# Kernel optimization log

Measured on AMD Instinct MI355X. Metric: run time of the kernel, lower is better.

The kernel has to match this reference:

```python
import jax, jax.numpy as jnp
from jax import lax
import numpy as np

ALPHA = 100.0  # NetVLAD beta

def _avg_pool2(x):
    # AvgPool2d(2, stride=2) on NCHW
    s = lax.reduce_window(x, 0.0, lax.add, (1, 1, 2, 2), (1, 1, 2, 2), 'VALID')
    return s * 0.25

def _conv3x3(x, w, b):
    y = lax.conv_general_dilated(x, w, (1, 1), 'SAME',
                                 dimension_numbers=('NCHW', 'OIHW', 'NCHW'))
    return y + b[None, :, None, None]

def _l2norm(v, axis):
    return v / jnp.maximum(jnp.linalg.norm(v, axis=axis, keepdims=True), 1e-12)


def setup_inputs() -> dict:
    key = jax.random.key(0)
    ks = jax.random.split(key, 10)
    N, H, W = 16, 512, 512
    K, D = 64, 16          # clusters, NetVLAD feature dim (conv2 out channels)
    T, E, Hd = 64, 300, 512  # caption len, emb dim (rnn_inp=rnn_out), rnn_hid
    img = jax.random.normal(ks[0], (N, 3, H, W), jnp.float32)
    cap = jax.random.normal(ks[1], (N, T, E), jnp.float32)
    conv1_w = jax.random.normal(ks[2], (4, 3, 3, 3), jnp.float32) * 0.1
    conv1_b = jnp.zeros((4,), jnp.float32)
    conv2_w = jax.random.normal(ks[3], (16, 4, 3, 3), jnp.float32) * 0.1
    conv2_b = jnp.zeros((16,), jnp.float32)
    centroids = jax.random.uniform(ks[4], (K, D), jnp.float32)  # torch.rand init
    nv_w = 2.0 * ALPHA * centroids                     # 1x1 conv weight, squeezed [K,D]
    nv_b = -ALPHA * jnp.linalg.norm(centroids, axis=1)  # [K]
    fc_w = jax.random.normal(ks[5], (Hd, K * D), jnp.float32) * 0.02
    fc_b = jnp.zeros((Hd,), jnp.float32)
    hid_w = jax.random.normal(ks[6], (Hd, E + Hd), jnp.float32) * 0.02
    hid_b = jnp.zeros((Hd,), jnp.float32)
    out_w = jax.random.normal(ks[7], (E, Hd), jnp.float32) * 0.02
    out_b = jnp.zeros((E,), jnp.float32)
    return dict(img=img, cap=cap, conv1_w=conv1_w, conv1_b=conv1_b,
                conv2_w=conv2_w, conv2_b=conv2_b, centroids=centroids,
                nv_w=nv_w, nv_b=nv_b, fc_w=fc_w, fc_b=fc_b,
                hid_w=hid_w, hid_b=hid_b, out_w=out_w, out_b=out_b)


def reference(img, cap, conv1_w, conv1_b, conv2_w, conv2_b, centroids,
              nv_w, nv_b, fc_w, fc_b, hid_w, hid_b, out_w, out_b):
    # CNN encoder
    x = jax.nn.relu(_conv3x3(img, conv1_w, conv1_b))
    x = _avg_pool2(x)
    x = jax.nn.relu(_conv3x3(x, conv2_w, conv2_b))
    x = _avg_pool2(x)                      # [N, 16, 128, 128]
    N, C = x.shape[0], x.shape[1]
    xf = x.reshape(N, C, -1)               # [N, C, HW]
    # NetVLAD: 1x1 conv -> softmax over clusters
    soft_assign = jnp.einsum('kc,nch->nkh', nv_w, xf) + nv_b[None, :, None]
    soft_assign = jax.nn.softmax(soft_assign, axis=1)  # [N, K, HW]
    # algebraic two-matmul form of sum_hw a[n,k,hw]*(x[n,c,hw]-centroids[k,c])
    a_sum = soft_assign.sum(axis=-1)                      # [N, K]
    vlad = jnp.einsum('nkh,nch->nkc', soft_assign, xf)    # [N, K, C]
    vlad = vlad - a_sum[:, :, None] * centroids[None]     # [N, K, C]
    vlad = _l2norm(vlad, axis=2)
    vlad = vlad.reshape(N, -1)
    vlad = _l2norm(vlad, axis=1)
    features = vlad @ fc_w.T + fc_b                        # [N, rnn_hid]
    # RNN decoder on sample 0
    feat0 = features[0]
    cap0 = cap[0]                                          # [T, E]

    def step(carry, x_t):
        h, x_in = carry
        comb = jnp.concatenate([x_in, h])
        h_new = jax.nn.sigmoid(hid_w @ comb + hid_b)
        y = jax.nn.sigmoid(out_w @ h_new + out_b)
        return (h_new, x_t), y

    (_, ys) = lax.scan(step, (feat0, cap0[0]), cap0[1:])
    output = jnp.concatenate([cap0[:1], ys], axis=0)       # [T, E]
    loss = jnp.mean((output - cap0) ** 2)
    return loss
```

## Files before the change

### kernel.cpp

```cpp
#include <hip/hip_runtime.h>
#include <math.h>


#define HPOISON 0xAAAAAAAAu

__device__ __forceinline__ float sigmoidf_(float x) {
  return 1.0f / (1.0f + __expf(-x));
}

__global__ __launch_bounds__(256) void k_conv1(const float* __restrict__ img,
                                               const float* __restrict__ w,
                                               const float* __restrict__ b,
                                               float* __restrict__ p1) {
  int idx = blockIdx.x * 256 + threadIdx.x;
  int ox = idx & 255;
  int oy = (idx >> 8) & 255;
  int c  = idx >> 16;
  __shared__ float wsh[27];
  __shared__ float bsh;
  if (threadIdx.x < 27) wsh[threadIdx.x] = w[c * 27 + threadIdx.x];
  if (threadIdx.x == 0) bsh = b[c];
  __syncthreads();
  int y0 = oy * 2 - 1, x0 = ox * 2 - 1;
  float a00, a01, a10, a11;
  a00 = a01 = a10 = a11 = bsh;
  #pragma unroll
  for (int ci = 0; ci < 3; ++ci) {
    float P[4][4];
    #pragma unroll
    for (int j = 0; j < 4; ++j) {
      int y = y0 + j;
      #pragma unroll
      for (int i = 0; i < 4; ++i) {
        int x = x0 + i;
        bool ok = ((unsigned)y < 512u) && ((unsigned)x < 512u);
        P[j][i] = ok ? img[ci * 262144 + y * 512 + x] : 0.0f;
      }
    }
    #pragma unroll
    for (int ky = 0; ky < 3; ++ky) {
      #pragma unroll
      for (int kx = 0; kx < 3; ++kx) {
        float wv = wsh[ci * 9 + ky * 3 + kx];
        a00 = fmaf(wv, P[ky][kx],         a00);
        a01 = fmaf(wv, P[ky][kx + 1],     a01);
        a10 = fmaf(wv, P[ky + 1][kx],     a10);
        a11 = fmaf(wv, P[ky + 1][kx + 1], a11);
      }
    }
  }
  p1[idx] = 0.25f * (fmaxf(a00, 0.f) + fmaxf(a01, 0.f) +
                     fmaxf(a10, 0.f) + fmaxf(a11, 0.f));
}

#define PS_STRIDE 65
#define XS_STRIDE 20
__global__ __launch_bounds__(256, 1) void k_conv2vlad(const float* __restrict__ p1,
                                                      const float* __restrict__ w2,
                                                      const float* __restrict__ b2,
                                                      const float* __restrict__ nvw,
                                                      const float* __restrict__ nvb,
                                                      float* __restrict__ vacc,
                                                      float* __restrict__ asum) {
  __shared__ __align__(16) float ps[128 * PS_STRIDE];
  __shared__ __align__(16) float xs[128 * XS_STRIDE];
  __shared__ float wsh[1024];
  __shared__ float bsh[64];
  __shared__ float aS[256];
  __shared__ float cw[576];
  __shared__ float cb[16];
  int tid = threadIdx.x;
  for (int i = tid; i < 1024; i += 256) wsh[i] = nvw[i];
  if (tid < 64) bsh[tid] = nvb[tid];
  for (int i = tid; i < 576; i += 256) cw[i] = w2[i];
  if (tid < 16) cb[tid] = b2[tid];
  __syncthreads();

  int ox = tid & 127;
  int oyl = tid >> 7;
  int oy = blockIdx.x * 2 + oyl;
  int y0 = oy * 2 - 1, x0 = ox * 2 - 1;
  float a[16][4];
  #pragma unroll
  for (int oc = 0; oc < 16; ++oc) {
    float bb = cb[oc];
    a[oc][0] = bb; a[oc][1] = bb; a[oc][2] = bb; a[oc][3] = bb;
  }
  #pragma unroll
  for (int ci = 0; ci < 4; ++ci) {
    float P[4][4];
    #pragma unroll
    for (int j = 0; j < 4; ++j) {
      int y = y0 + j;
      #pragma unroll
      for (int i = 0; i < 4; ++i) {
        int x = x0 + i;
        bool ok = ((unsigned)y < 256u) && ((unsigned)x < 256u);
        P[j][i] = ok ? p1[ci * 65536 + y * 256 + x] : 0.0f;
      }
    }
    #pragma unroll
    for (int oc = 0; oc < 16; ++oc) {
      #pragma unroll
      for (int ky = 0; ky < 3; ++ky) {
        #pragma unroll
        for (int kx = 0; kx < 3; ++kx) {
          float wv = cw[oc * 36 + ci * 9 + ky * 3 + kx];
          a[oc][0] = fmaf(wv, P[ky][kx],         a[oc][0]);
          a[oc][1] = fmaf(wv, P[ky][kx + 1],     a[oc][1]);
          a[oc][2] = fmaf(wv, P[ky + 1][kx],     a[oc][2]);
          a[oc][3] = fmaf(wv, P[ky + 1][kx + 1], a[oc][3]);
        }
      }
    }
  }
  float x[16];
  #pragma unroll
  for (int oc = 0; oc < 16; ++oc)
    x[oc] = 0.25f * (fmaxf(a[oc][0], 0.f) + fmaxf(a[oc][1], 0.f) +
                     fmaxf(a[oc][2], 0.f) + fmaxf(a[oc][3], 0.f));

  float p[64];
  float m = -1e30f;
  #pragma unroll
  for (int k = 0; k < 64; ++k) {
    float acc = bsh[k];
    #pragma unroll
    for (int c = 0; c < 16; ++c) acc = fmaf(wsh[k * 16 + c], x[c], acc);
    p[k] = acc;
    m = fmaxf(m, acc);
  }
  float s = 0.f;
  #pragma unroll
  for (int k = 0; k < 64; ++k) { p[k] = __expf(p[k] - m); s += p[k]; }
  float inv = 1.0f / s;
  #pragma unroll
  for (int k = 0; k < 64; ++k) p[k] *= inv;

  int q = tid >> 6, k = tid & 63;
  float acc[16];
  #pragma unroll
  for (int c = 0; c < 16; ++c) acc[c] = 0.f;
  float accA = 0.f;

  for (int pass = 0; pass < 2; ++pass) {
    __syncthreads();
    if ((tid >> 7) == pass) {
      int tt = tid & 127;
      #pragma unroll
      for (int kk = 0; kk < 64; ++kk) ps[tt * PS_STRIDE + kk] = p[kk];
      #pragma unroll
      for (int c = 0; c < 16; ++c) xs[tt * XS_STRIDE + c] = x[c];
    }
    __syncthreads();
    #pragma unroll
    for (int j = 0; j < 32; ++j) {
      int tt = q * 32 + j;
      float pv = ps[tt * PS_STRIDE + k];
      accA += pv;
      const float4* xv = (const float4*)(xs + tt * XS_STRIDE);
      #pragma unroll
      for (int c4 = 0; c4 < 4; ++c4) {
        float4 xx = xv[c4];
        acc[c4 * 4 + 0] = fmaf(pv, xx.x, acc[c4 * 4 + 0]);
        acc[c4 * 4 + 1] = fmaf(pv, xx.y, acc[c4 * 4 + 1]);
        acc[c4 * 4 + 2] = fmaf(pv, xx.z, acc[c4 * 4 + 2]);
        acc[c4 * 4 + 3] = fmaf(pv, xx.w, acc[c4 * 4 + 3]);
      }
    }
  }
  __syncthreads();
  float* red = ps;
  #pragma unroll
  for (int c = 0; c < 16; ++c) red[tid * 16 + c] = acc[c];
  aS[tid] = accA;
  __syncthreads();
  if (q == 0) {
    float aa = aS[k] + aS[64 + k] + aS[128 + k] + aS[192 + k];
    atomicAdd(&asum[k], aa);
  }
  int k2 = tid >> 2;
  int cg = (tid & 3) * 4;
  #pragma unroll
  for (int cc = 0; cc < 4; ++cc) {
    int c = cg + cc;
    float v = red[(0 * 64 + k2) * 16 + c] + red[(1 * 64 + k2) * 16 + c] +
              red[(2 * 64 + k2) * 16 + c] + red[(3 * 64 + k2) * 16 + c];
    atomicAdd(&vacc[k2 * 16 + c], v);
  }
}

__global__ __launch_bounds__(512) void k_featU(const float* __restrict__ hid_w,
                                               const float* __restrict__ hid_b,
                                               const float* __restrict__ cap,
                                               const float* __restrict__ vacc,
                                               const float* __restrict__ asum,
                                               const float* __restrict__ cent,
                                               const float* __restrict__ fcw,
                                               const float* __restrict__ fcb,
                                               float* __restrict__ U,
                                               float* __restrict__ feat) {
  int tid = threadIdx.x;
  if (blockIdx.x < 63) {
    int t = blockIdx.x;
    __shared__ __align__(16) float csh[300];
    if (tid < 300) csh[tid] = cap[t * 300 + tid];
    __syncthreads();
    float acc = hid_b[tid];
    const float4* w4 = (const float4*)(hid_w + tid * 812);
    const float4* c4 = (const float4*)csh;
    #pragma unroll 5
    for (int i = 0; i < 75; ++i) {
      float4 aa = w4[i]; float4 xx = c4[i];
      acc = fmaf(aa.x, xx.x, acc); acc = fmaf(aa.y, xx.y, acc);
      acc = fmaf(aa.z, xx.z, acc); acc = fmaf(aa.w, xx.w, acc);
    }
    U[t * 512 + tid] = acc;
    return;
  }
  int q = blockIdx.x - 63;
  __shared__ __align__(16) float v[1024];
  __shared__ float rn[64];
  __shared__ float red[9];
  for (int i = tid; i < 1024; i += 512)
    v[i] = vacc[i] - asum[i >> 4] * cent[i];
  __syncthreads();
  if (tid < 64) {
    float ss = 0.f;
    #pragma unroll
    for (int c = 0; c < 16; ++c) { float xx = v[tid * 16 + c]; ss = fmaf(xx, xx, ss); }
    rn[tid] = fmaxf(sqrtf(ss), 1e-12f);
  }
  __syncthreads();
  float gs = 0.f;
  for (int i = tid; i < 1024; i += 512) {
    float nv = v[i] / rn[i >> 4];
    v[i] = nv;
    gs = fmaf(nv, nv, gs);
  }
  #pragma unroll
  for (int o = 32; o > 0; o >>= 1) gs += __shfl_down(gs, o);
  int wv = tid >> 6, lane = tid & 63;
  if (lane == 0) red[wv] = gs;
  __syncthreads();
  if (tid == 0) {
    float tot = 0.f;
    #pragma unroll
    for (int qq = 0; qq < 8; ++qq) tot += red[qq];
    red[8] = 1.0f / fmaxf(sqrtf(tot), 1e-12f);
  }
  __syncthreads();
  float invg = red[8];
  int r = q * 64 + (tid >> 3);
  int cch = tid & 7;
  float acc = 0.f;
  const float4* fw4 = (const float4*)(fcw + r * 1024 + cch * 128);
  const float4* v4  = (const float4*)(v + cch * 128);
  #pragma unroll 4
  for (int i = 0; i < 32; ++i) {
    float4 aa = fw4[i]; float4 xx = v4[i];
    acc = fmaf(aa.x, xx.x, acc); acc = fmaf(aa.y, xx.y, acc);
    acc = fmaf(aa.z, xx.z, acc); acc = fmaf(aa.w, xx.w, acc);
  }
  acc += __shfl_down(acc, 4, 8);
  acc += __shfl_down(acc, 2, 8);
  acc += __shfl_down(acc, 1, 8);
  if (cch == 0) feat[r] = fmaf(invg, acc, fcb[r]);
}

__global__ __launch_bounds__(256, 1) void k_rnn(const float* __restrict__ hid_w,
                                                const float* __restrict__ U,
                                                const float* __restrict__ feat,
                                                float* __restrict__ H) {
  const int b = blockIdx.x;
  const int tid = threadIdx.x;
  const int wv = tid >> 6;
  const int lane = tid & 63;
  const int row = b * 64 + lane;
  const int colbase = wv * 128;
  float4 wr[32];
  const float4* wp = (const float4*)(hid_w + row * 812 + 300 + colbase);
  #pragma unroll
  for (int i = 0; i < 32; ++i) wr[i] = wp[i];
  __shared__ __align__(16) float hsh[512];
  __shared__ float part[4][64];
  unsigned int* Hu = (unsigned int*)H;
  for (int t = 0; t < 63; ++t) {
    float uval = (wv == 0) ? U[t * 512 + row] : 0.f;
    if (t == 0) {
      hsh[tid] = feat[tid];
      hsh[tid + 256] = feat[tid + 256];
    } else {
      const unsigned int* src = Hu + (t - 1) * 512;
      unsigned int a0, a1;
      do {
        a0 = __hip_atomic_load(src + tid, __ATOMIC_RELAXED,
                               __HIP_MEMORY_SCOPE_AGENT);
      } while (a0 == HPOISON);
      do {
        a1 = __hip_atomic_load(src + tid + 256, __ATOMIC_RELAXED,
                               __HIP_MEMORY_SCOPE_AGENT);
      } while (a1 == HPOISON);
      hsh[tid] = __uint_as_float(a0);
      hsh[tid + 256] = __uint_as_float(a1);
    }
    __syncthreads();
    float acc = 0.0f;
    #pragma unroll
    for (int i = 0; i < 32; ++i) {
      float4 hv = *(const float4*)(hsh + colbase + i * 4);
      acc = fmaf(wr[i].x, hv.x, acc);
      acc = fmaf(wr[i].y, hv.y, acc);
      acc = fmaf(wr[i].z, hv.z, acc);
      acc = fmaf(wr[i].w, hv.w, acc);
    }
    part[wv][lane] = acc;
    __syncthreads();
    if (wv == 0) {
      float pre = part[0][lane] + part[1][lane] + part[2][lane] +
                  part[3][lane] + uval;
      float hn = sigmoidf_(pre);
      __hip_atomic_store(Hu + t * 512 + row, __float_as_uint(hn),
                         __ATOMIC_RELAXED, __HIP_MEMORY_SCOPE_AGENT);
    }
  }
}

__global__ __launch_bounds__(512) void k_loss(const float* __restrict__ outw,
                                              const float* __restrict__ outb,
                                              const float* __restrict__ H,
                                              const float* __restrict__ cap,
                                              float* __restrict__ loss) {
  int t = blockIdx.x;
  int tid = threadIdx.x;
  __shared__ __align__(16) float hsh[512];
  __shared__ float red[8];
  hsh[tid] = H[t * 512 + tid];
  __syncthreads();
  float se = 0.f;
  if (tid < 300) {
    float acc = outb[tid];
    const float4* w4 = (const float4*)(outw + tid * 512);
    const float4* h4 = (const float4*)hsh;
    #pragma unroll 4
    for (int i = 0; i < 128; ++i) {
      float4 aa = w4[i]; float4 xx = h4[i];
      acc = fmaf(aa.x, xx.x, acc); acc = fmaf(aa.y, xx.y, acc);
      acc = fmaf(aa.z, xx.z, acc); acc = fmaf(aa.w, xx.w, acc);
    }
    float y = sigmoidf_(acc);
    float d = y - cap[(t + 1) * 300 + tid];
    se = d * d;
  }
  #pragma unroll
  for (int o = 32; o > 0; o >>= 1) se += __shfl_down(se, o);
  if ((tid & 63) == 0) red[tid >> 6] = se;
  __syncthreads();
  if (tid == 0) {
    float tot = 0.f;
    #pragma unroll
    for (int qq = 0; qq < 8; ++qq) tot += red[qq];
    atomicAdd(loss, tot * (1.0f / 19200.0f));
  }
}

extern "C" void kernel_launch(void* const* d_in, const int* in_sizes, int n_in,
                              void* d_out, int out_size, void* d_ws, size_t ws_size,
                              hipStream_t stream) {
  (void)in_sizes; (void)n_in; (void)out_size; (void)ws_size;
  const float* img  = (const float*)d_in[0];
  const float* cap  = (const float*)d_in[1];
  const float* c1w  = (const float*)d_in[2];
  const float* c1b  = (const float*)d_in[3];
  const float* c2w  = (const float*)d_in[4];
  const float* c2b  = (const float*)d_in[5];
  const float* cent = (const float*)d_in[6];
  const float* nvw  = (const float*)d_in[7];
  const float* nvb  = (const float*)d_in[8];
  const float* fcw  = (const float*)d_in[9];
  const float* fcb  = (const float*)d_in[10];
  const float* hidw = (const float*)d_in[11];
  const float* hidb = (const float*)d_in[12];
  const float* outw = (const float*)d_in[13];
  const float* outb = (const float*)d_in[14];

  float* ws   = (float*)d_ws;
  float* p1   = ws;
  float* vacc = ws + 262144;
  float* asum = ws + 263168;
  float* feat = ws + 263232;
  float* U    = ws + 263744;
  float* H    = ws + 296000;

  hipMemsetAsync(vacc, 0, (1024 + 64) * sizeof(float), stream);
  hipMemsetAsync(H, 0xAA, 63 * 512 * sizeof(float), stream);
  hipMemsetAsync(d_out, 0, sizeof(float), stream);

  k_conv1<<<1024, 256, 0, stream>>>(img, c1w, c1b, p1);
  k_conv2vlad<<<64, 256, 0, stream>>>(p1, c2w, c2b, nvw, nvb, vacc, asum);
  k_featU<<<71, 512, 0, stream>>>(hidw, hidb, cap, vacc, asum, cent,
                                  fcw, fcb, U, feat);
  k_rnn<<<8, 256, 0, stream>>>(hidw, U, feat, H);
  k_loss<<<63, 512, 0, stream>>>(outw, outb, H, cap, (float*)d_out);
}
```

Before: 296.2 us.

## Fold memsets and U precompute into conv1 launch; make RNN step wave-local

The three memset calls and the caption-side U projection move into extra blocks of the conv1 kernel, which removes separate launches and overlaps the U work with the convolution. The old featU kernel shrinks to just the FC part. The RNN kernel now has each wave own 16 rows, with 4 lanes per row splitting the columns. Each wave keeps its own copy of h and reduces with shuffles, so the block-level __syncthreads and the shared partial-sum exchange are replaced by wave barriers. The cost is redundant polling of H by every wave and wider per-lane atomic loads.

```diff
diff --git a/kernel.cpp b/kernel.cpp
--- a/kernel.cpp
+++ b/kernel.cpp
@@ -8,49 +8,90 @@
   return 1.0f / (1.0f + __expf(-x));
 }
 
-__global__ __launch_bounds__(256) void k_conv1(const float* __restrict__ img,
+__global__ __launch_bounds__(256) void k_front(const float* __restrict__ img,
                                                const float* __restrict__ w,
                                                const float* __restrict__ b,
-                                               float* __restrict__ p1) {
-  int idx = blockIdx.x * 256 + threadIdx.x;
-  int ox = idx & 255;
-  int oy = (idx >> 8) & 255;
-  int c  = idx >> 16;
-  __shared__ float wsh[27];
-  __shared__ float bsh;
-  if (threadIdx.x < 27) wsh[threadIdx.x] = w[c * 27 + threadIdx.x];
-  if (threadIdx.x == 0) bsh = b[c];
-  __syncthreads();
-  int y0 = oy * 2 - 1, x0 = ox * 2 - 1;
-  float a00, a01, a10, a11;
-  a00 = a01 = a10 = a11 = bsh;
-  #pragma unroll
-  for (int ci = 0; ci < 3; ++ci) {
-    float P[4][4];
-    #pragma unroll
-    for (int j = 0; j < 4; ++j) {
-      int y = y0 + j;
-      #pragma unroll
-      for (int i = 0; i < 4; ++i) {
-        int x = x0 + i;
-        bool ok = ((unsigned)y < 512u) && ((unsigned)x < 512u);
-        P[j][i] = ok ? img[ci * 262144 + y * 512 + x] : 0.0f;
-      }
-    }
-    #pragma unroll
-    for (int ky = 0; ky < 3; ++ky) {
-      #pragma unroll
-      for (int kx = 0; kx < 3; ++kx) {
-        float wv = wsh[ci * 9 + ky * 3 + kx];
-        a00 = fmaf(wv, P[ky][kx],         a00);
-        a01 = fmaf(wv, P[ky][kx + 1],     a01);
-        a10 = fmaf(wv, P[ky + 1][kx],     a10);
-        a11 = fmaf(wv, P[ky + 1][kx + 1], a11);
-      }
-    }
-  }
-  p1[idx] = 0.25f * (fmaxf(a00, 0.f) + fmaxf(a01, 0.f) +
-                     fmaxf(a10, 0.f) + fmaxf(a11, 0.f));
+                                               const float* __restrict__ hid_w,
+                                               const float* __restrict__ hid_b,
+                                               const float* __restrict__ cap,
+                                               float* __restrict__ p1,
+                                               float* __restrict__ U,
+                                               float* __restrict__ vacc,
+                                               float* __restrict__ asum,
+                                               float* __restrict__ H,
+                                               float* __restrict__ out) {
+  int bx = blockIdx.x;
+  int tid = threadIdx.x;
+  if (bx < 1024) {
+    int idx = bx * 256 + tid;
+    int ox = idx & 255;
+    int oy = (idx >> 8) & 255;
+    int c  = idx >> 16;
+    __shared__ float wsh[27];
+    __shared__ float bsh;
+    if (tid < 27) wsh[tid] = w[c * 27 + tid];
+    if (tid == 0) bsh = b[c];
+    __syncthreads();
+    int y0 = oy * 2 - 1, x0 = ox * 2 - 1;
+    float a00, a01, a10, a11;
+    a00 = a01 = a10 = a11 = bsh;
+    #pragma unroll
+    for (int ci = 0; ci < 3; ++ci) {
+      float P[4][4];
+      #pragma unroll
+      for (int j = 0; j < 4; ++j) {
+        int y = y0 + j;
+        #pragma unroll
+        for (int i = 0; i < 4; ++i) {
+          int x = x0 + i;
+          bool ok = ((unsigned)y < 512u) && ((unsigned)x < 512u);
+          P[j][i] = ok ? img[ci * 262144 + y * 512 + x] : 0.0f;
+        }
+      }
+      #pragma unroll
+      for (int ky = 0; ky < 3; ++ky) {
+        #pragma unroll
+        for (int kx = 0; kx < 3; ++kx) {
+          float wv = wsh[ci * 9 + ky * 3 + kx];
+          a00 = fmaf(wv, P[ky][kx],         a00);
+          a01 = fmaf(wv, P[ky][kx + 1],     a01);
+          a10 = fmaf(wv, P[ky + 1][kx],     a10);
+          a11 = fmaf(wv, P[ky + 1][kx + 1], a11);
+        }
+      }
+    }
+    p1[idx] = 0.25f * (fmaxf(a00, 0.f) + fmaxf(a01, 0.f) +
+                       fmaxf(a10, 0.f) + fmaxf(a11, 0.f));
+    return;
+  }
+  if (bx < 1087) {
+    int t = bx - 1024;
+    __shared__ __align__(16) float csh[300];
+    if (tid < 256) csh[tid] = cap[t * 300 + tid];
+    if (tid < 44) csh[256 + tid] = cap[t * 300 + 256 + tid];
+    __syncthreads();
+    #pragma unroll
+    for (int rr = 0; rr < 2; ++rr) {
+      int r = tid + rr * 256;
+      float acc = hid_b[r];
+      const float4* w4 = (const float4*)(hid_w + r * 812);
+      const float4* c4 = (const float4*)csh;
+      #pragma unroll 5
+      for (int i = 0; i < 75; ++i) {
+        float4 aa = w4[i]; float4 xx = c4[i];
+        acc = fmaf(aa.x, xx.x, acc); acc = fmaf(aa.y, xx.y, acc);
+        acc = fmaf(aa.z, xx.z, acc); acc = fmaf(aa.w, xx.w, acc);
+      }
+      U[t * 512 + r] = acc;
+    }
+    return;
+  }
+  for (int i = tid; i < 1024; i += 256) vacc[i] = 0.f;
+  if (tid < 64) asum[tid] = 0.f;
+  if (tid == 0) out[0] = 0.f;
+  uint4* Hu4 = (uint4*)H;
+  uint4 pz = make_uint4(HPOISON, HPOISON, HPOISON, HPOISON);
+  for (int i = tid; i < (63 * 512) / 4; i += 256) Hu4[i] = pz;
 }
 
 #define PS_STRIDE 65
@@ -190,35 +231,14 @@
   }
 }
 
-__global__ __launch_bounds__(512) void k_featU(const float* __restrict__ hid_w,
-                                               const float* __restrict__ hid_b,
-                                               const float* __restrict__ cap,
-                                               const float* __restrict__ vacc,
-                                               const float* __restrict__ asum,
-                                               const float* __restrict__ cent,
-                                               const float* __restrict__ fcw,
-                                               const float* __restrict__ fcb,
-                                               float* __restrict__ U,
-                                               float* __restrict__ feat) {
+__global__ __launch_bounds__(512) void k_fc(const float* __restrict__ vacc,
+                                            const float* __restrict__ asum,
+                                            const float* __restrict__ cent,
+                                            const float* __restrict__ fcw,
+                                            const float* __restrict__ fcb,
+                                            float* __restrict__ feat) {
   int tid = threadIdx.x;
-  if (blockIdx.x < 63) {
-    int t = blockIdx.x;
-    __shared__ __align__(16) float csh[300];
-    if (tid < 300) csh[tid] = cap[t * 300 + tid];
-    __syncthreads();
-    float acc = hid_b[tid];
-    const float4* w4 = (const float4*)(hid_w + tid * 812);
-    const float4* c4 = (const float4*)csh;
-    #pragma unroll 5
-    for (int i = 0; i < 75; ++i) {
-      float4 aa = w4[i]; float4 xx = c4[i];
-      acc = fmaf(aa.x, xx.x, acc); acc = fmaf(aa.y, xx.y, acc);
-      acc = fmaf(aa.z, xx.z, acc); acc = fmaf(aa.w, xx.w, acc);
-    }
-    U[t * 512 + tid] = acc;
-    return;
-  }
-  int q = blockIdx.x - 63;
+  int q = blockIdx.x;
   __shared__ __align__(16) float v[1024];
   __shared__ float rn[64];
   __shared__ float red[9];
@@ -272,57 +292,61 @@
                                                 const float* __restrict__ U,
                                                 const float* __restrict__ feat,
                                                 float* __restrict__ H) {
-  const int b = blockIdx.x;
   const int tid = threadIdx.x;
   const int wv = tid >> 6;
   const int lane = tid & 63;
-  const int row = b * 64 + lane;
-  const int colbase = wv * 128;
+  const int r = lane >> 2;
+  const int cg = lane & 3;
+  const int row = blockIdx.x * 64 + wv * 16 + r;
+  const int colbase = cg * 128;
   float4 wr[32];
   const float4* wp = (const float4*)(hid_w + row * 812 + 300 + colbase);
   #pragma unroll
   for (int i = 0; i < 32; ++i) wr[i] = wp[i];
-  __shared__ __align__(16) float hsh[512];
-  __shared__ float part[4][64];
+  __shared__ __align__(16) float hsh[4][512];
+  float* hw = hsh[wv];
   unsigned int* Hu = (unsigned int*)H;
+  const int pbase = lane * 8;
   for (int t = 0; t < 63; ++t) {
-    float uval = (wv == 0) ? U[t * 512 + row] : 0.f;
+    float uval = U[t * 512 + row];
     if (t == 0) {
-      hsh[tid] = feat[tid];
-      hsh[tid + 256] = feat[tid + 256];
+      float4 f0 = *(const float4*)(feat + pbase);
+      float4 f1 = *(const float4*)(feat + pbase + 4);
+      *(float4*)(hw + pbase) = f0;
+      *(float4*)(hw + pbase + 4) = f1;
     } else {
-      const unsigned int* src = Hu + (t - 1) * 512;
-      unsigned int a0, a1;
+      const unsigned int* src = Hu + (t - 1) * 512 + pbase;
+      unsigned int a[8];
+      bool again;
       do {
-        a0 = __hip_atomic_load(src + tid, __ATOMIC_RELAXED,
-                               __HIP_MEMORY_SCOPE_AGENT);
-      } while (a0 == HPOISON);
-      do {
-        a1 = __hip_atomic_load(src + tid + 256, __ATOMIC_RELAXED,
-                               __HIP_MEMORY_SCOPE_AGENT);
-      } while (a1 == HPOISON);
-      hsh[tid] = __uint_as_float(a0);
-      hsh[tid + 256] = __uint_as_float(a1);
-    }
-    __syncthreads();
+        #pragma unroll
+        for (int j = 0; j < 8; ++j)
+          a[j] = __hip_atomic_load(src + j, __ATOMIC_RELAXED,
+                                   __HIP_MEMORY_SCOPE_AGENT);
+        again = false;
+        #pragma unroll
+        for (int j = 0; j < 8; ++j) again = again || (a[j] == HPOISON);
+      } while (again);
+      #pragma unroll
+      for (int j = 0; j < 8; ++j) hw[pbase + j] = __uint_as_float(a[j]);
+    }
+    __builtin_amdgcn_wave_barrier();
     float acc = 0.0f;
     #pragma unroll
     for (int i = 0; i < 32; ++i) {
-      float4 hv = *(const float4*)(hsh + colbase + i * 4);
+      float4 hv = *(const float4*)(hw + colbase + i * 4);
       acc = fmaf(wr[i].x, hv.x, acc);
       acc = fmaf(wr[i].y, hv.y, acc);
       acc = fmaf(wr[i].z, hv.z, acc);
       acc = fmaf(wr[i].w, hv.w, acc);
     }
-    part[wv][lane] = acc;
-    __syncthreads();
-    if (wv == 0) {
-      float pre = part[0][lane] + part[1][lane] + part[2][lane] +
-                  part[3][lane] + uval;
-      float hn = sigmoidf_(pre);
+    acc += __shfl_xor(acc, 1);
+    acc += __shfl_xor(acc, 2);
+    float hn = sigmoidf_(acc + uval);
+    if (cg == 0)
       __hip_atomic_store(Hu + t * 512 + row, __float_as_uint(hn),
                          __ATOMIC_RELAXED, __HIP_MEMORY_SCOPE_AGENT);
-    }
+    __builtin_amdgcn_wave_barrier();
   }
 }
 
@@ -392,14 +416,10 @@
   float* U    = ws + 263744;
   float* H    = ws + 296000;
 
-  hipMemsetAsync(vacc, 0, (1024 + 64) * sizeof(float), stream);
-  hipMemsetAsync(H, 0xAA, 63 * 512 * sizeof(float), stream);
-  hipMemsetAsync(d_out, 0, sizeof(float), stream);
-
-  k_conv1<<<1024, 256, 0, stream>>>(img, c1w, c1b, p1);
+  k_front<<<1088, 256, 0, stream>>>(img, c1w, c1b, hidw, hidb, cap,
+                                    p1, U, vacc, asum, H, (float*)d_out);
   k_conv2vlad<<<64, 256, 0, stream>>>(p1, c2w, c2b, nvw, nvb, vacc, asum);
-  k_featU<<<71, 512, 0, stream>>>(hidw, hidb, cap, vacc, asum, cent,
-                                  fcw, fcb, U, feat);
+  k_fc<<<8, 512, 0, stream>>>(vacc, asum, cent, fcw, fcb, feat);
   k_rnn<<<8, 256, 0, stream>>>(hidw, U, feat, H);
   k_loss<<<63, 512, 0, stream>>>(outw, outb, H, cap, (float*)d_out);
 }
```

New measurement: 391.2 us. 32.1% more time.

## Fuse whole pipeline into one persistent kernel with flag-based inter-block sync

Applied to the files above, without the earlier changes.

Replaces the three memsets and five kernel launches with a single 256-block persistent kernel whose blocks take different roles: conv1 workers, conv2+VLAD workers, feature projection, input projection, RNN recurrence and loss. Ordering between roles uses a magic ready flag, completion counters, and poison-value polling on global buffers in place of kernel boundaries. This removes launch and memset overhead and lets the U-projection and loss work overlap the serial RNN. In exchange it depends on every block being co-resident, since spinning blocks would otherwise deadlock, and the flag protocol is fragile because the magic flag is never reset between calls.

```diff
diff --git a/kernel.cpp b/kernel.cpp
--- a/kernel.cpp
+++ b/kernel.cpp
@@ -2,365 +2,446 @@
 #include <math.h>
 
 
-#define HPOISON 0xAAAAAAAAu
+#define POISON 0xAAAAAAAAu
+#define MAGIC  0x13579BDFu
 
 __device__ __forceinline__ float sigmoidf_(float x) {
   return 1.0f / (1.0f + __expf(-x));
 }
-
-__global__ __launch_bounds__(256) void k_conv1(const float* __restrict__ img,
-                                               const float* __restrict__ w,
-                                               const float* __restrict__ b,
-                                               float* __restrict__ p1) {
-  int idx = blockIdx.x * 256 + threadIdx.x;
-  int ox = idx & 255;
-  int oy = (idx >> 8) & 255;
-  int c  = idx >> 16;
-  __shared__ float wsh[27];
-  __shared__ float bsh;
-  if (threadIdx.x < 27) wsh[threadIdx.x] = w[c * 27 + threadIdx.x];
-  if (threadIdx.x == 0) bsh = b[c];
-  __syncthreads();
-  int y0 = oy * 2 - 1, x0 = ox * 2 - 1;
-  float a00, a01, a10, a11;
-  a00 = a01 = a10 = a11 = bsh;
-  #pragma unroll
-  for (int ci = 0; ci < 3; ++ci) {
-    float P[4][4];
-    #pragma unroll
-    for (int j = 0; j < 4; ++j) {
-      int y = y0 + j;
-      #pragma unroll
-      for (int i = 0; i < 4; ++i) {
-        int x = x0 + i;
-        bool ok = ((unsigned)y < 512u) && ((unsigned)x < 512u);
-        P[j][i] = ok ? img[ci * 262144 + y * 512 + x] : 0.0f;
-      }
-    }
-    #pragma unroll
-    for (int ky = 0; ky < 3; ++ky) {
-      #pragma unroll
-      for (int kx = 0; kx < 3; ++kx) {
-        float wv = wsh[ci * 9 + ky * 3 + kx];
-        a00 = fmaf(wv, P[ky][kx],         a00);
-        a01 = fmaf(wv, P[ky][kx + 1],     a01);
-        a10 = fmaf(wv, P[ky + 1][kx],     a10);
-        a11 = fmaf(wv, P[ky + 1][kx + 1], a11);
-      }
-    }
+__device__ __forceinline__ unsigned uld(const unsigned* p) {
+  return __hip_atomic_load(p, __ATOMIC_RELAXED, __HIP_MEMORY_SCOPE_AGENT);
+}
+__device__ __forceinline__ float fld(const float* p) {
+  return __hip_atomic_load(p, __ATOMIC_RELAXED, __HIP_MEMORY_SCOPE_AGENT);
+}
+__device__ __forceinline__ void fst(float* p, float v) {
+  __hip_atomic_store(p, v, __ATOMIC_RELAXED, __HIP_MEMORY_SCOPE_AGENT);
+}
+__device__ __forceinline__ void ust(unsigned* p, unsigned v) {
+  __hip_atomic_store(p, v, __ATOMIC_RELAXED, __HIP_MEMORY_SCOPE_AGENT);
+}
+
+__global__ __launch_bounds__(256, 1)
+void k_fused(const float* __restrict__ img,  const float* __restrict__ cap,
+             const float* __restrict__ c1w,  const float* __restrict__ c1b,
+             const float* __restrict__ c2w,  const float* __restrict__ c2b,
+             const float* __restrict__ cent, const float* __restrict__ nvw,
+             const float* __restrict__ nvb,  const float* __restrict__ fcw,
+             const float* __restrict__ fcb,  const float* __restrict__ hidw,
+             const float* __restrict__ hidb, const float* __restrict__ outw,
+             const float* __restrict__ outb,
+             float* __restrict__ p1,   float* __restrict__ vacc,
+             float* __restrict__ asum, float* __restrict__ feat,
+             float* __restrict__ U,    float* __restrict__ H,
+             unsigned* __restrict__ flags, float* __restrict__ loss) {
+  __shared__ __align__(16) float smem[12832];
+  const int bx  = blockIdx.x;
+  const int tid = threadIdx.x;
+  unsigned* flag_ready = flags + 0;
+  unsigned* conv_done  = flags + 1;
+  unsigned* vlad_done  = flags + 2;
+
+  if (bx < 8) {
+    if (bx == 0) {
+      for (int i = tid; i < 1024; i += 256) fst(vacc + i, 0.f);
+      if (tid < 64) fst(asum + tid, 0.f);
+      if (tid == 0) { fst(loss, 0.f); ust(conv_done, 0u); ust(vlad_done, 0u); }
+      unsigned* Uu = (unsigned*)U;
+      unsigned* Hu = (unsigned*)H;
+      unsigned* Fu = (unsigned*)feat;
+      for (int i = tid; i < 63 * 512; i += 256) ust(Uu + i, POISON);
+      for (int i = tid; i < 63 * 512; i += 256) ust(Hu + i, POISON);
+      if (tid < 256) { ust(Fu + tid, POISON); ust(Fu + tid + 256, POISON); }
+      __syncthreads();
+      if (tid == 0)
+        __hip_atomic_store(flag_ready, MAGIC, __ATOMIC_RELEASE,
+                           __HIP_MEMORY_SCOPE_AGENT);
+    }
+    const int r   = tid >> 2;
+    const int cg  = tid & 3;
+    const int row = bx * 64 + r;
+    float4 wr[32];
+    const float4* wp = (const float4*)(hidw + row * 812 + 300 + cg * 128);
+    #pragma unroll
+    for (int i = 0; i < 32; ++i) wr[i] = wp[i];
+    if (bx != 0) {
+      if (tid == 0) {
+        while (__hip_atomic_load(flag_ready, __ATOMIC_ACQUIRE,
+                                 __HIP_MEMORY_SCOPE_AGENT) != MAGIC)
+          __builtin_amdgcn_s_sleep(2);
+      }
+      __syncthreads();
+    }
+    float* buf0 = smem;
+    float* buf1 = smem + 544;
+    const int w0 = (tid >> 7) * 136 + (tid & 127);
+    const int w1 = ((tid + 256) >> 7) * 136 + ((tid + 256) & 127);
+    const int wown = (row >> 7) * 136 + (row & 127);
+    const bool own0 = ((tid >> 6) == bx);
+    const bool own1 = (((tid + 256) >> 6) == bx);
+    {
+      const unsigned* fu = (const unsigned*)feat;
+      unsigned f0, f1;
+      do {
+        f0 = uld(fu + tid);
+        f1 = uld(fu + tid + 256);
+      } while (f0 == POISON || f1 == POISON);
+      buf0[w0] = __uint_as_float(f0);
+      buf0[w1] = __uint_as_float(f1);
+    }
+    unsigned upat = 0;
+    if (cg == 0) upat = uld((const unsigned*)(U + row));
+    __syncthreads();
+    unsigned* Hu = (unsigned*)H;
+    for (int t = 0; t < 63; ++t) {
+      const float* bufc = (t & 1) ? buf1 : buf0;
+      const float* rb = bufc + cg * 136;
+      float acc = 0.f;
+      #pragma unroll
+      for (int i = 0; i < 32; ++i) {
+        float4 h4 = *(const float4*)(rb + i * 4);
+        acc = fmaf(wr[i].x, h4.x, acc);
+        acc = fmaf(wr[i].y, h4.y, acc);
+        acc = fmaf(wr[i].z, h4.z, acc);
+        acc = fmaf(wr[i].w, h4.w, acc);
+      }
+      acc += __shfl_xor(acc, 1);
+      acc += __shfl_xor(acc, 2);
+      float hn = 0.f;
+      if (cg == 0) {
+        while (upat == POISON) upat = uld((const unsigned*)(U + t * 512 + row));
+        hn = sigmoidf_(acc + __uint_as_float(upat));
+        fst(H + t * 512 + row, hn);
+      }
+      if (t < 62) {
+        float* bufn = (t & 1) ? buf0 : buf1;
+        if (cg == 0) {
+          bufn[wown] = hn;
+          upat = uld((const unsigned*)(U + (t + 1) * 512 + row));
+        }
+        const unsigned* src = Hu + t * 512;
+        unsigned a0 = 0, a1 = 0;
+        do {
+          if (!own0) a0 = uld(src + tid);
+          if (!own1) a1 = uld(src + tid + 256);
+        } while ((!own0 && a0 == POISON) || (!own1 && a1 == POISON));
+        if (!own0) bufn[w0] = __uint_as_float(a0);
+        if (!own1) bufn[w1] = __uint_as_float(a1);
+        __syncthreads();
+      }
+    }
+    return;
   }
-  p1[idx] = 0.25f * (fmaxf(a00, 0.f) + fmaxf(a01, 0.f) +
-                     fmaxf(a10, 0.f) + fmaxf(a11, 0.f));
-}
-
-#define PS_STRIDE 65
-#define XS_STRIDE 20
-__global__ __launch_bounds__(256, 1) void k_conv2vlad(const float* __restrict__ p1,
-                                                      const float* __restrict__ w2,
-                                                      const float* __restrict__ b2,
-                                                      const float* __restrict__ nvw,
-                                                      const float* __restrict__ nvb,
-                                                      float* __restrict__ vacc,
-                                                      float* __restrict__ asum) {
-  __shared__ __align__(16) float ps[128 * PS_STRIDE];
-  __shared__ __align__(16) float xs[128 * XS_STRIDE];
-  __shared__ float wsh[1024];
-  __shared__ float bsh[64];
-  __shared__ float aS[256];
-  __shared__ float cw[576];
-  __shared__ float cb[16];
-  int tid = threadIdx.x;
-  for (int i = tid; i < 1024; i += 256) wsh[i] = nvw[i];
-  if (tid < 64) bsh[tid] = nvb[tid];
-  for (int i = tid; i < 576; i += 256) cw[i] = w2[i];
-  if (tid < 16) cb[tid] = b2[tid];
-  __syncthreads();
-
-  int ox = tid & 127;
-  int oyl = tid >> 7;
-  int oy = blockIdx.x * 2 + oyl;
-  int y0 = oy * 2 - 1, x0 = ox * 2 - 1;
-  float a[16][4];
-  #pragma unroll
-  for (int oc = 0; oc < 16; ++oc) {
-    float bb = cb[oc];
-    a[oc][0] = bb; a[oc][1] = bb; a[oc][2] = bb; a[oc][3] = bb;
+
+  if (bx < 71) {
+    const int t = bx - 8;
+    if (tid == 0) {
+      while (__hip_atomic_load(flag_ready, __ATOMIC_ACQUIRE,
+                               __HIP_MEMORY_SCOPE_AGENT) != MAGIC)
+        __builtin_amdgcn_s_sleep(8);
+    }
+    __syncthreads();
+    float* csh = smem;
+    if (tid < 256) csh[tid] = cap[t * 300 + tid];
+    if (tid < 44) csh[256 + tid] = cap[t * 300 + 256 + tid];
+    __syncthreads();
+    #pragma unroll
+    for (int rr = 0; rr < 2; ++rr) {
+      int rrow = tid + rr * 256;
+      float acc = hidb[rrow];
+      const float4* w4 = (const float4*)(hidw + rrow * 812);
+      const float4* c4 = (const float4*)csh;
+      #pragma unroll 5
+      for (int i = 0; i < 75; ++i) {
+        float4 aa = w4[i]; float4 xx = c4[i];
+        acc = fmaf(aa.x, xx.x, acc); acc = fmaf(aa.y, xx.y, acc);
+        acc = fmaf(aa.z, xx.z, acc); acc = fmaf(aa.w, xx.w, acc);
+      }
+      fst(U + t * 512 + rrow, acc);
+    }
+    __syncthreads();
+    const unsigned* Hu = (const unsigned*)H;
+    if (tid == 0) {
+      while (uld(Hu + (size_t)t * 512) == POISON) __builtin_amdgcn_s_sleep(64);
+    }
+    __syncthreads();
+    float* hsh = smem;
+    {
+      const unsigned* src = Hu + (size_t)t * 512;
+      unsigned a0, a1;
+      do {
+        a0 = uld(src + tid);
+        a1 = uld(src + tid + 256);
+      } while (a0 == POISON || a1 == POISON);
+      hsh[tid] = __uint_as_float(a0);
+      hsh[tid + 256] = __uint_as_float(a1);
+    }
+    __syncthreads();
+    float se = 0.f;
+    #pragma unroll
+    for (int rr = 0; rr < 2; ++rr) {
+      int orow = tid + rr * 256;
+      if (orow < 300) {
+        float acc = outb[orow];
+        const float4* w4 = (const float4*)(outw + orow * 512);
+        const float4* h4 = (const float4*)hsh;
+        #pragma unroll 4
+        for (int i = 0; i < 128; ++i) {
+          float4 aa = w4[i]; float4 xx = h4[i];
+          acc = fmaf(aa.x, xx.x, acc); acc = fmaf(aa.y, xx.y, acc);
+          acc = fmaf(aa.z, xx.z, acc); acc = fmaf(aa.w, xx.w, acc);
+        }
+        float y = sigmoidf_(acc);
+        float d = y - cap[(t + 1) * 300 + orow];
+        se = fmaf(d, d, se);
+      }
+    }
+    #pragma unroll
+    for (int o = 32; o > 0; o >>= 1) se += __shfl_down(se, o);
+    float* red = smem + 512;
+    if ((tid & 63) == 0) red[tid >> 6] = se;
+    __syncthreads();
+    if (tid == 0) {
+      float tot = red[0] + red[1] + red[2] + red[3];
+      atomicAdd(loss, tot * (1.0f / 19200.0f));
+    }
+    return;
   }
-  #pragma unroll
-  for (int ci = 0; ci < 4; ++ci) {
-    float P[4][4];
-    #pragma unroll
-    for (int j = 0; j < 4; ++j) {
-      int y = y0 + j;
-      #pragma unroll
-      for (int i = 0; i < 4; ++i) {
-        int x = x0 + i;
-        bool ok = ((unsigned)y < 256u) && ((unsigned)x < 256u);
-        P[j][i] = ok ? p1[ci * 65536 + y * 256 + x] : 0.0f;
-      }
-    }
-    #pragma unroll
-    for (int oc = 0; oc < 16; ++oc) {
-      #pragma unroll
-      for (int ky = 0; ky < 3; ++ky) {
-        #pragma unroll
-        for (int kx = 0; kx < 3; ++kx) {
-          float wv = cw[oc * 36 + ci * 9 + ky * 3 + kx];
-          a[oc][0] = fmaf(wv, P[ky][kx],         a[oc][0]);
-          a[oc][1] = fmaf(wv, P[ky][kx + 1],     a[oc][1]);
-          a[oc][2] = fmaf(wv, P[ky + 1][kx],     a[oc][2]);
-          a[oc][3] = fmaf(wv, P[ky + 1][kx + 1], a[oc][3]);
-        }
-      }
-    }
-  }
-  float x[16];
-  #pragma unroll
-  for (int oc = 0; oc < 16; ++oc)
-    x[oc] = 0.25f * (fmaxf(a[oc][0], 0.f) + fmaxf(a[oc][1], 0.f) +
-                     fmaxf(a[oc][2], 0.f) + fmaxf(a[oc][3], 0.f));
-
-  float p[64];
-  float m = -1e30f;
-  #pragma unroll
-  for (int k = 0; k < 64; ++k) {
-    float acc = bsh[k];
-    #pragma unroll
-    for (int c = 0; c < 16; ++c) acc = fmaf(wsh[k * 16 + c], x[c], acc);
-    p[k] = acc;
-    m = fmaxf(m, acc);
-  }
-  float s = 0.f;
-  #pragma unroll
-  for (int k = 0; k < 64; ++k) { p[k] = __expf(p[k] - m); s += p[k]; }
-  float inv = 1.0f / s;
-  #pragma unroll
-  for (int k = 0; k < 64; ++k) p[k] *= inv;
-
-  int q = tid >> 6, k = tid & 63;
-  float acc[16];
-  #pragma unroll
-  for (int c = 0; c < 16; ++c) acc[c] = 0.f;
-  float accA = 0.f;
-
-  for (int pass = 0; pass < 2; ++pass) {
-    __syncthreads();
-    if ((tid >> 7) == pass) {
-      int tt = tid & 127;
-      #pragma unroll
-      for (int kk = 0; kk < 64; ++kk) ps[tt * PS_STRIDE + kk] = p[kk];
-      #pragma unroll
-      for (int c = 0; c < 16; ++c) xs[tt * XS_STRIDE + c] = x[c];
-    }
-    __syncthreads();
-    #pragma unroll
-    for (int j = 0; j < 32; ++j) {
-      int tt = q * 32 + j;
-      float pv = ps[tt * PS_STRIDE + k];
-      accA += pv;
-      const float4* xv = (const float4*)(xs + tt * XS_STRIDE);
-      #pragma unroll
-      for (int c4 = 0; c4 < 4; ++c4) {
-        float4 xx = xv[c4];
-        acc[c4 * 4 + 0] = fmaf(pv, xx.x, acc[c4 * 4 + 0]);
-        acc[c4 * 4 + 1] = fmaf(pv, xx.y, acc[c4 * 4 + 1]);
-        acc[c4 * 4 + 2] = fmaf(pv, xx.z, acc[c4 * 4 + 2]);
-        acc[c4 * 4 + 3] = fmaf(pv, xx.w, acc[c4 * 4 + 3]);
-      }
-    }
-  }
-  __syncthreads();
-  float* red = ps;
-  #pragma unroll
-  for (int c = 0; c < 16; ++c) red[tid * 16 + c] = acc[c];
-  aS[tid] = accA;
-  __syncthreads();
-  if (q == 0) {
-    float aa = aS[k] + aS[64 + k] + aS[128 + k] + aS[192 + k];
-    atomicAdd(&asum[k], aa);
-  }
-  int k2 = tid >> 2;
-  int cg = (tid & 3) * 4;
-  #pragma unroll
-  for (int cc = 0; cc < 4; ++cc) {
-    int c = cg + cc;
-    float v = red[(0 * 64 + k2) * 16 + c] + red[(1 * 64 + k2) * 16 + c] +
-              red[(2 * 64 + k2) * 16 + c] + red[(3 * 64 + k2) * 16 + c];
-    atomicAdd(&vacc[k2 * 16 + c], v);
-  }
-}
-
-__global__ __launch_bounds__(512) void k_featU(const float* __restrict__ hid_w,
-                                               const float* __restrict__ hid_b,
-                                               const float* __restrict__ cap,
-                                               const float* __restrict__ vacc,
-                                               const float* __restrict__ asum,
-                                               const float* __restrict__ cent,
-                                               const float* __restrict__ fcw,
-                                               const float* __restrict__ fcb,
-                                               float* __restrict__ U,
-                                               float* __restrict__ feat) {
-  int tid = threadIdx.x;
-  if (blockIdx.x < 63) {
-    int t = blockIdx.x;
-    __shared__ __align__(16) float csh[300];
-    if (tid < 300) csh[tid] = cap[t * 300 + tid];
-    __syncthreads();
-    float acc = hid_b[tid];
-    const float4* w4 = (const float4*)(hid_w + tid * 812);
-    const float4* c4 = (const float4*)csh;
-    #pragma unroll 5
-    for (int i = 0; i < 75; ++i) {
-      float4 aa = w4[i]; float4 xx = c4[i];
+
+  if (bx < 79) {
+    const int q = bx - 71;
+    if (tid == 0) {
+      while (uld(vlad_done) != 64u) __builtin_amdgcn_s_sleep(8);
+    }
+    __syncthreads();
+    float* v  = smem;
+    float* rn = smem + 1024;
+    float* fr = smem + 1088;
+    for (int i = tid; i < 1024; i += 256)
+      v[i] = fld(vacc + i) - fld(asum + (i >> 4)) * cent[i];
+    __syncthreads();
+    if (tid < 64) {
+      float ss = 0.f;
+      #pragma unroll
+      for (int c = 0; c < 16; ++c) { float xx = v[tid * 16 + c]; ss = fmaf(xx, xx, ss); }
+      rn[tid] = fmaxf(sqrtf(ss), 1e-12f);
+    }
+    __syncthreads();
+    float gs = 0.f;
+    for (int i = tid; i < 1024; i += 256) {
+      float nv = v[i] / rn[i >> 4];
+      v[i] = nv;
+      gs = fmaf(nv, nv, gs);
+    }
+    #pragma unroll
+    for (int o = 32; o > 0; o >>= 1) gs += __shfl_down(gs, o);
+    if ((tid & 63) == 0) fr[tid >> 6] = gs;
+    __syncthreads();
+    if (tid == 0) {
+      float tot = fr[0] + fr[1] + fr[2] + fr[3];
+      fr[8] = 1.0f / fmaxf(sqrtf(tot), 1e-12f);
+    }
+    __syncthreads();
+    float invg = fr[8];
+    int row = q * 64 + (tid >> 2);
+    int cg = tid & 3;
+    float acc = 0.f;
+    const float4* fw4 = (const float4*)(fcw + row * 1024 + cg * 256);
+    const float4* v4  = (const float4*)(v + cg * 256);
+    #pragma unroll 4
+    for (int i = 0; i < 64; ++i) {
+      float4 aa = fw4[i]; float4 xx = v4[i];
       acc = fmaf(aa.x, xx.x, acc); acc = fmaf(aa.y, xx.y, acc);
       acc = fmaf(aa.z, xx.z, acc); acc = fmaf(aa.w, xx.w, acc);
     }
-    U[t * 512 + tid] = acc;
+    acc += __shfl_xor(acc, 1);
+    acc += __shfl_xor(acc, 2);
+    if (cg == 0) fst(feat + row, fmaf(invg, acc, fcb[row]));
     return;
   }
-  int q = blockIdx.x - 63;
-  __shared__ __align__(16) float v[1024];
-  __shared__ float rn[64];
-  __shared__ float red[9];
-  for (int i = tid; i < 1024; i += 512)
-    v[i] = vacc[i] - asum[i >> 4] * cent[i];
-  __syncthreads();
-  if (tid < 64) {
-    float ss = 0.f;
-    #pragma unroll
-    for (int c = 0; c < 16; ++c) { float xx = v[tid * 16 + c]; ss = fmaf(xx, xx, ss); }
-    rn[tid] = fmaxf(sqrtf(ss), 1e-12f);
+
+  if (bx < 143) {
+    const int vb = bx - 79;
+    float* ps  = smem;
+    float* xs  = smem + 8320;
+    float* wsh = smem + 10880;
+    float* bsh = smem + 11904;
+    float* aS  = smem + 11968;
+    float* cw  = smem + 12224;
+    float* cb  = smem + 12800;
+    for (int i = tid; i < 1024; i += 256) wsh[i] = nvw[i];
+    if (tid < 64) bsh[tid] = nvb[tid];
+    for (int i = tid; i < 576; i += 256) cw[i] = c2w[i];
+    if (tid < 16) cb[tid] = c2b[tid];
+    if (tid == 0) {
+      while (uld(conv_done) != 113u) __builtin_amdgcn_s_sleep(4);
+    }
+    __syncthreads();
+    int ox = tid & 127;
+    int oy = vb * 2 + (tid >> 7);
+    int y0 = oy * 2 - 1, x0 = ox * 2 - 1;
+    float a[16][4];
+    #pragma unroll
+    for (int oc = 0; oc < 16; ++oc) {
+      float bb = cb[oc];
+      a[oc][0] = bb; a[oc][1] = bb; a[oc][2] = bb; a[oc][3] = bb;
+    }
+    #pragma unroll
+    for (int ci = 0; ci < 4; ++ci) {
+      float P[4][4];
+      #pragma unroll
+      for (int j = 0; j < 4; ++j) {
+        int y = y0 + j;
+        #pragma unroll
+        for (int i = 0; i < 4; ++i) {
+          int x = x0 + i;
+          bool ok = ((unsigned)y < 256u) && ((unsigned)x < 256u);
+          P[j][i] = ok ? fld(p1 + ci * 65536 + y * 256 + x) : 0.0f;
+        }
+      }
+      #pragma unroll
+      for (int oc = 0; oc < 16; ++oc) {
+        #pragma unroll
+        for (int ky = 0; ky < 3; ++ky) {
+          #pragma unroll
+          for (int kx = 0; kx < 3; ++kx) {
+            float wv = cw[oc * 36 + ci * 9 + ky * 3 + kx];
+            a[oc][0] = fmaf(wv, P[ky][kx],         a[oc][0]);
+            a[oc][1] = fmaf(wv, P[ky][kx + 1],     a[oc][1]);
+            a[oc][2] = fmaf(wv, P[ky + 1][kx],     a[oc][2]);
+            a[oc][3] = fmaf(wv, P[ky + 1][kx + 1], a[oc][3]);
+          }
+        }
+      }
+    }
+    float x[16];
+    #pragma unroll
+    for (int oc = 0; oc < 16; ++oc)
+      x[oc] = 0.25f * (fmaxf(a[oc][0], 0.f) + fmaxf(a[oc][1], 0.f) +
+                       fmaxf(a[oc][2], 0.f) + fmaxf(a[oc][3], 0.f));
+    float p[64];
+    float m = -1e30f;
+    #pragma unroll
+    for (int k = 0; k < 64; ++k) {
+      float acc = bsh[k];
+      #pragma unroll
+      for (int c = 0; c < 16; ++c) acc = fmaf(wsh[k * 16 + c], x[c], acc);
+      p[k] = acc;
+      m = fmaxf(m, acc);
+    }
+    float s = 0.f;
+    #pragma unroll
+    for (int k = 0; k < 64; ++k) { p[k] = __expf(p[k] - m); s += p[k]; }
+    float inv = 1.0f / s;
+    #pragma unroll
+    for (int k = 0; k < 64; ++k) p[k] *= inv;
+
+    int q = tid >> 6, k = tid & 63;
+    float acc[16];
+    #pragma unroll
+    for (int c = 0; c < 16; ++c) acc[c] = 0.f;
+    float accA = 0.f;
+    for (int pass = 0; pass < 2; ++pass) {
+      __syncthreads();
+      if ((tid >> 7) == pass) {
+        int tt = tid & 127;
+        #pragma unroll
+        for (int kk = 0; kk < 64; ++kk) ps[tt * 65 + kk] = p[kk];
+        #pragma unroll
+        for (int c = 0; c < 16; ++c) xs[tt * 20 + c] = x[c];
+      }
+      __syncthreads();
+      #pragma unroll
+      for (int j = 0; j < 32; ++j) {
+        int tt = q * 32 + j;
+        float pv = ps[tt * 65 + k];
+        accA += pv;
+        const float4* xv = (const float4*)(xs + tt * 20);
+        #pragma unroll
+        for (int c4 = 0; c4 < 4; ++c4) {
+          float4 xx = xv[c4];
+          acc[c4 * 4 + 0] = fmaf(pv, xx.x, acc[c4 * 4 + 0]);
+          acc[c4 * 4 + 1] = fmaf(pv, xx.y, acc[c4 * 4 + 1]);
+          acc[c4 * 4 + 2] = fmaf(pv, xx.z, acc[c4 * 4 + 2]);
+          acc[c4 * 4 + 3] = fmaf(pv, xx.w, acc[c4 * 4 + 3]);
+        }
+      }
+    }
+    __syncthreads();
+    float* red = ps;
+    #pragma unroll
+    for (int c = 0; c < 16; ++c) red[tid * 16 + c] = acc[c];
+    aS[tid] = accA;
+    __syncthreads();
+    if (q == 0) {
+      float aa = aS[k] + aS[64 + k] + aS[128 + k] + aS[192 + k];
+      atomicAdd(&asum[k], aa);
+    }
+    int k2 = tid >> 2;
+    int cgc = (tid & 3) * 4;
+    #pragma unroll
+    for (int cc = 0; cc < 4; ++cc) {
+      int c = cgc + cc;
+      float vv = red[(0 * 64 + k2) * 16 + c] + red[(1 * 64 + k2) * 16 + c] +
+                 red[(2 * 64 + k2) * 16 + c] + red[(3 * 64 + k2) * 16 + c];
+      atomicAdd(&vacc[k2 * 16 + c], vv);
+    }
+    __syncthreads();
+    if (tid == 0)
+      __hip_atomic_fetch_add(vlad_done, 1u, __ATOMIC_RELAXED,
+                             __HIP_MEMORY_SCOPE_AGENT);
+    return;
   }
-  __syncthreads();
-  float gs = 0.f;
-  for (int i = tid; i < 1024; i += 512) {
-    float nv = v[i] / rn[i >> 4];
-    v[i] = nv;
-    gs = fmaf(nv, nv, gs);
-  }
-  #pragma unroll
-  for (int o = 32; o > 0; o >>= 1) gs += __shfl_down(gs, o);
-  int wv = tid >> 6, lane = tid & 63;
-  if (lane == 0) red[wv] = gs;
-  __syncthreads();
-  if (tid == 0) {
-    float tot = 0.f;
-    #pragma unroll
-    for (int qq = 0; qq < 8; ++qq) tot += red[qq];
-    red[8] = 1.0f / fmaxf(sqrtf(tot), 1e-12f);
-  }
-  __syncthreads();
-  float invg = red[8];
-  int r = q * 64 + (tid >> 3);
-  int cch = tid & 7;
-  float acc = 0.f;
-  const float4* fw4 = (const float4*)(fcw + r * 1024 + cch * 128);
-  const float4* v4  = (const float4*)(v + cch * 128);
-  #pragma unroll 4
-  for (int i = 0; i < 32; ++i) {
-    float4 aa = fw4[i]; float4 xx = v4[i];
-    acc = fmaf(aa.x, xx.x, acc); acc = fmaf(aa.y, xx.y, acc);
-    acc = fmaf(aa.z, xx.z, acc); acc = fmaf(aa.w, xx.w, acc);
-  }
-  acc += __shfl_down(acc, 4, 8);
-  acc += __shfl_down(acc, 2, 8);
-  acc += __shfl_down(acc, 1, 8);
-  if (cch == 0) feat[r] = fmaf(invg, acc, fcb[r]);
-}
-
-__global__ __launch_bounds__(256, 1) void k_rnn(const float* __restrict__ hid_w,
-                                                const float* __restrict__ U,
-                                                const float* __restrict__ feat,
-                                                float* __restrict__ H) {
-  const int b = blockIdx.x;
-  const int tid = threadIdx.x;
-  const int wv = tid >> 6;
-  const int lane = tid & 63;
-  const int row = b * 64 + lane;
-  const int colbase = wv * 128;
-  float4 wr[32];
-  const float4* wp = (const float4*)(hid_w + row * 812 + 300 + colbase);
-  #pragma unroll
-  for (int i = 0; i < 32; ++i) wr[i] = wp[i];
-  __shared__ __align__(16) float hsh[512];
-  __shared__ float part[4][64];
-  unsigned int* Hu = (unsigned int*)H;
-  for (int t = 0; t < 63; ++t) {
-    float uval = (wv == 0) ? U[t * 512 + row] : 0.f;
-    if (t == 0) {
-      hsh[tid] = feat[tid];
-      hsh[tid + 256] = feat[tid + 256];
-    } else {
-      const unsigned int* src = Hu + (t - 1) * 512;
-      unsigned int a0, a1;
-      do {
-        a0 = __hip_atomic_load(src + tid, __ATOMIC_RELAXED,
-                               __HIP_MEMORY_SCOPE_AGENT);
-      } while (a0 == HPOISON);
-      do {
-        a1 = __hip_atomic_load(src + tid + 256, __ATOMIC_RELAXED,
-                               __HIP_MEMORY_SCOPE_AGENT);
-      } while (a1 == HPOISON);
-      hsh[tid] = __uint_as_float(a0);
-      hsh[tid + 256] = __uint_as_float(a1);
-    }
-    __syncthreads();
-    float acc = 0.0f;
-    #pragma unroll
-    for (int i = 0; i < 32; ++i) {
-      float4 hv = *(const float4*)(hsh + colbase + i * 4);
-      acc = fmaf(wr[i].x, hv.x, acc);
-      acc = fmaf(wr[i].y, hv.y, acc);
-      acc = fmaf(wr[i].z, hv.z, acc);
-      acc = fmaf(wr[i].w, hv.w, acc);
-    }
-    part[wv][lane] = acc;
-    __syncthreads();
-    if (wv == 0) {
-      float pre = part[0][lane] + part[1][lane] + part[2][lane] +
-                  part[3][lane] + uval;
-      float hn = sigmoidf_(pre);
-      __hip_atomic_store(Hu + t * 512 + row, __float_as_uint(hn),
-                         __ATOMIC_RELAXED, __HIP_MEMORY_SCOPE_AGENT);
-    }
-  }
-}
-
-__global__ __launch_bounds__(512) void k_loss(const float* __restrict__ outw,
-                                              const float* __restrict__ outb,
-                                              const float* __restrict__ H,
-                                              const float* __restrict__ cap,
-                                              float* __restrict__ loss) {
-  int t = blockIdx.x;
-  int tid = threadIdx.x;
-  __shared__ __align__(16) float hsh[512];
-  __shared__ float red[8];
-  hsh[tid] = H[t * 512 + tid];
-  __syncthreads();
-  float se = 0.f;
-  if (tid < 300) {
-    float acc = outb[tid];
-    const float4* w4 = (const float4*)(outw + tid * 512);
-    const float4* h4 = (const float4*)hsh;
-    #pragma unroll 4
-    for (int i = 0; i < 128; ++i) {
-      float4 aa = w4[i]; float4 xx = h4[i];
-      acc = fmaf(aa.x, xx.x, acc); acc = fmaf(aa.y, xx.y, acc);
-      acc = fmaf(aa.z, xx.z, acc); acc = fmaf(aa.w, xx.w, acc);
-    }
-    float y = sigmoidf_(acc);
-    float d = y - cap[(t + 1) * 300 + tid];
-    se = d * d;
-  }
-  #pragma unroll
-  for (int o = 32; o > 0; o >>= 1) se += __shfl_down(se, o);
-  if ((tid & 63) == 0) red[tid >> 6] = se;
-  __syncthreads();
-  if (tid == 0) {
-    float tot = 0.f;
-    #pragma unroll
-    for (int qq = 0; qq < 8; ++qq) tot += red[qq];
-    atomicAdd(loss, tot * (1.0f / 19200.0f));
+
+  {
+    const int cbk = bx - 143;
+    float* cwsh = smem;
+    if (tid < 108) cwsh[tid] = c1w[tid];
+    if (tid < 4) cwsh[108 + tid] = c1b[tid];
+    __syncthreads();
+    for (int o = cbk * 256 + tid; o < 262144; o += 113 * 256) {
+      int c  = o >> 16;
+      int oy = (o >> 8) & 255;
+      int ox = o & 255;
+      int y0 = oy * 2 - 1, x0 = ox * 2 - 1;
+      float a00, a01, a10, a11;
+      a00 = a01 = a10 = a11 = cwsh[108 + c];
+      #pragma unroll
+      for (int ci = 0; ci < 3; ++ci) {
+        float P[4][4];
+        #pragma unroll
+        for (int j = 0; j < 4; ++j) {
+          int y = y0 + j;
+          #pragma unroll
+          for (int i = 0; i < 4; ++i) {
+            int x = x0 + i;
+            bool ok = ((unsigned)y < 512u) && ((unsigned)x < 512u);
+            P[j][i] = ok ? img[ci * 262144 + y * 512 + x] : 0.0f;
+          }
+        }
+        #pragma unroll
+        for (int ky = 0; ky < 3; ++ky) {
+          #pragma unroll
+          for (int kx = 0; kx < 3; ++kx) {
+            float wv = cwsh[c * 27 + ci * 9 + ky * 3 + kx];
+            a00 = fmaf(wv, P[ky][kx],         a00);
+            a01 = fmaf(wv, P[ky][kx + 1],     a01);
+            a10 = fmaf(wv, P[ky + 1][kx],     a10);
+            a11 = fmaf(wv, P[ky + 1][kx + 1], a11);
+          }
+        }
+      }
+      fst(p1 + o, 0.25f * (fmaxf(a00, 0.f) + fmaxf(a01, 0.f) +
+                           fmaxf(a10, 0.f) + fmaxf(a11, 0.f)));
+    }
+    __syncthreads();
+    if (tid == 0) {
+      while (__hip_atomic_load(flag_ready, __ATOMIC_ACQUIRE,
+                               __HIP_MEMORY_SCOPE_AGENT) != MAGIC)
+        __builtin_amdgcn_s_sleep(2);
+      __hip_atomic_fetch_add(conv_done, 1u, __ATOMIC_RELAXED,
+                             __HIP_MEMORY_SCOPE_AGENT);
+    }
   }
 }
 
@@ -391,15 +472,10 @@
   float* feat = ws + 263232;
   float* U    = ws + 263744;
   float* H    = ws + 296000;
-
-  hipMemsetAsync(vacc, 0, (1024 + 64) * sizeof(float), stream);
-  hipMemsetAsync(H, 0xAA, 63 * 512 * sizeof(float), stream);
-  hipMemsetAsync(d_out, 0, sizeof(float), stream);
-
-  k_conv1<<<1024, 256, 0, stream>>>(img, c1w, c1b, p1);
-  k_conv2vlad<<<64, 256, 0, stream>>>(p1, c2w, c2b, nvw, nvb, vacc, asum);
-  k_featU<<<71, 512, 0, stream>>>(hidw, hidb, cap, vacc, asum, cent,
-                                  fcw, fcb, U, feat);
-  k_rnn<<<8, 256, 0, stream>>>(hidw, U, feat, H);
-  k_loss<<<63, 512, 0, stream>>>(outw, outb, H, cap, (float*)d_out);
-}
+  unsigned* flags = (unsigned*)(ws + 328256);
+
+  k_fused<<<256, 256, 0, stream>>>(img, cap, c1w, c1b, c2w, c2b, cent, nvw,
+                                   nvb, fcw, fcb, hidw, hidb, outw, outb,
+                                   p1, vacc, asum, feat, U, H, flags,
+                                   (float*)d_out);
+}
```

Result: no change. 293.4 us (-0.9%).
